# Optimization experiments

Hardware: AMD Instinct MI355X
Metric: run time of the kernel (lower is better)

Reference implementation:

```python
import jax, jax.numpy as jnp
import numpy as np

EPS = 1e-5  # torch BatchNorm1d default eps


def setup_inputs() -> dict:
    key = jax.random.key(0)
    ks = jax.random.split(key, 4)
    B, D, H, T = 1024, 256, 1024, 128
    s_ih = 1.0 / np.sqrt(H)
    return {
        "x": jax.random.normal(ks[0], (B, D), dtype=jnp.float32),
        "h0": jnp.zeros((B, H), dtype=jnp.float32),
        "W_ih": jax.random.normal(ks[1], (3 * H, D), dtype=jnp.float32) * s_ih,
        "W_hh": jax.random.normal(ks[2], (3 * H, H), dtype=jnp.float32) * s_ih,
        "b_ih": jnp.zeros((3 * H,), dtype=jnp.float32),
        "b_hh": jnp.zeros((3 * H,), dtype=jnp.float32),
        "W_lin": jax.random.normal(ks[3], (D, H), dtype=jnp.float32) * s_ih,
        "b_lin": jnp.zeros((D,), dtype=jnp.float32),
        "n_frames": T,
    }


def reference(x, h0, W_ih, W_hh, b_ih, b_hh, W_lin, b_lin, n_frames):
    H = h0.shape[-1]

    def step(carry, _):
        h, inp = carry
        gi = inp @ W_ih.T + b_ih          # (B, 3H)
        gh = h @ W_hh.T + b_hh            # (B, 3H)
        i_r, i_z, i_n = jnp.split(gi, 3, axis=-1)
        h_r, h_z, h_n = jnp.split(gh, 3, axis=-1)
        r = jax.nn.sigmoid(i_r + h_r)
        z = jax.nn.sigmoid(i_z + h_z)
        n = jnp.tanh(i_n + r * h_n)
        h_new = (1.0 - z) * n + z * h
        out = h_new @ W_lin.T + b_lin     # (B, D) -> next input
        return (h_new, out), out

    _, outs = jax.lax.scan(step, (h0, x), None, length=n_frames)  # (T, B, D)

    # BatchNorm1d(affine=False), training mode: per-frame batch statistics
    mean = outs.mean(axis=1, keepdims=True)
    var = outs.var(axis=1, keepdims=True)  # biased variance, as torch BN uses
    return (outs - mean) * jax.lax.rsqrt(var + EPS)
```

## Files before the change

kernel.cpp:

```cpp
#include <hip/hip_runtime.h>


#define DEVI __device__ __forceinline__

typedef __bf16 bf16x8 __attribute__((ext_vector_type(8)));
typedef float f32x4 __attribute__((ext_vector_type(4)));
typedef unsigned int u32x4 __attribute__((ext_vector_type(4)));

typedef __attribute__((address_space(1))) const unsigned int g_u32;
typedef __attribute__((address_space(3))) unsigned int l_u32;

DEVI unsigned short f2b(float f) {
  union { float f; unsigned u; } v; v.f = f;
  return (unsigned short)((v.u + 0x7fffu + ((v.u >> 16) & 1u)) >> 16);
}

DEVI void gl_lds16(const void* g, void* s) {
  __builtin_amdgcn_global_load_lds((g_u32*)g, (l_u32*)s, 16, 0, 0);
}
DEVI void st16_sc1(void* p, u32x4 v) {
  asm volatile("global_store_dwordx4 %0, %1, off sc1"
               :: "v"((unsigned long long)(__SIZE_TYPE__)p), "v"(v) : "memory");
}

DEVI float sigm(float x) { return 1.0f / (1.0f + __expf(-x)); }
DEVI float tanh_f(float x) {
  float t = __expf(-2.0f * fabsf(x));
  float r = (1.0f - t) / (1.0f + t);
  return x >= 0.0f ? r : -r;
}

__global__ __launch_bounds__(256, 2) void gru_persist(
    const unsigned short* __restrict__ XB,
    const unsigned short* __restrict__ WP0,
    const unsigned short* __restrict__ WP,
    const float* __restrict__ C0v,
    const float* __restrict__ CBv,
    const float* __restrict__ h0,
    unsigned short* __restrict__ HH,
    unsigned int* __restrict__ bar)
{
  __shared__ __align__(16) unsigned short As[3][64 * 64];
  __shared__ __align__(16) unsigned short Bs[3][128 * 64];
  __shared__ __align__(16) unsigned short Hs[64 * 32];
  const int tid = threadIdx.x;
  const int w = tid >> 6, lane = tid & 63;
  const int wr = w >> 1, wc = w & 1;
  const int srow = lane >> 3;
  const int schunk = (lane & 7) ^ srow;
  const int l15 = lane & 15, lg = lane >> 4;
  const int xb_ = blockIdx.x & 7, rb_ = blockIdx.x >> 3;
  const int mb = (xb_ >> 2) | ((rb_ & 7) << 1);
  const int nb = (xb_ & 3) | ((rb_ >> 3) << 2);
  const int j = nb * 32 + wc * 16 + l15;

  const float c0r = C0v[j], c0z = C0v[1024 + j], c0i = C0v[2048 + j], c0h = C0v[3072 + j];
  const float cbr = CBv[j], cbz = CBv[1024 + j], cbi = CBv[2048 + j], cbh = CBv[3072 + j];

  float hreg[2][4];
#pragma unroll
  for (int mi = 0; mi < 2; ++mi)
#pragma unroll
    for (int i = 0; i < 4; ++i)
      hreg[mi][i] = h0[(size_t)(mb * 64 + wr * 32 + mi * 16 + lg * 4 + i) * 1024 + j];

  int offA[2][2], offB[2][4];
#pragma unroll
  for (int kk = 0; kk < 2; ++kk) {
#pragma unroll
    for (int mi = 0; mi < 2; ++mi) {
      int rl = wr * 32 + mi * 16 + l15;
      int slot = (kk * 4 + lg) ^ (rl & 7);
      offA[kk][mi] = rl * 128 + slot * 16;
    }
#pragma unroll
    for (int g = 0; g < 4; ++g) {
      int cl = wc * 64 + g * 16 + l15;
      int slot = (kk * 4 + lg) ^ (cl & 7);
      offB[kk][g] = cl * 128 + slot * 16;
    }
  }
  const int offq0 = (0 * 8 + srow) * 1024 + schunk * 8;
  const int offq1 = (1 * 8 + srow) * 1024 + schunk * 8;
  const int offq2 = (2 * 8 + srow) * 1024 + schunk * 8;
  const int offq3 = (3 * 8 + srow) * 1024 + schunk * 8;
  const size_t arow_off = (size_t)(mb * 64 + w * 16) * 1024;
  const unsigned short* BrowS = WP + (size_t)(nb * 128 + w * 32) * 1024;
  const unsigned short* Arow0 = XB + (size_t)(mb * 64 + w * 16) * 256;
  const unsigned short* Brow0 = WP0 + (size_t)(nb * 128 + w * 32) * 256;

#define STAGE0(KT, BUF)                                                       \
  _Pragma("unroll")                                                           \
  for (int q = 0; q < 4; ++q)                                                 \
    gl_lds16(Brow0 + (size_t)(q * 8 + srow) * 256 + (KT) * 64 + schunk * 8,   \
             (char*)Bs[BUF] + (w * 32 + q * 8) * 128);                        \
  _Pragma("unroll")                                                           \
  for (int q = 0; q < 2; ++q)                                                 \
    gl_lds16(Arow0 + (size_t)(q * 8 + srow) * 256 + (KT) * 64 + schunk * 8,   \
             (char*)As[BUF] + (w * 16 + q * 8) * 128);
#define SSTAGE_B(KT, BUF)                                                     \
  gl_lds16(BrowS + offq0 + (KT) * 64, (char*)Bs[BUF] + (w * 32) * 128);       \
  gl_lds16(BrowS + offq1 + (KT) * 64, (char*)Bs[BUF] + (w * 32 + 8) * 128);   \
  gl_lds16(BrowS + offq2 + (KT) * 64, (char*)Bs[BUF] + (w * 32 + 16) * 128);  \
  gl_lds16(BrowS + offq3 + (KT) * 64, (char*)Bs[BUF] + (w * 32 + 24) * 128);
#define SSTAGE_A(KT, BUF)                                                     \
  gl_lds16(ArowS + offq0 + (KT) * 64, (char*)As[BUF] + (w * 16) * 128);       \
  gl_lds16(ArowS + offq1 + (KT) * 64, (char*)As[BUF] + (w * 16 + 8) * 128);

  for (int t = 0; t < 128; ++t) {
    const bool first = (t == 0);
    const int iters = first ? 4 : 16;
    const unsigned short* ArowS =
        HH + (((size_t)(first ? 0 : t - 1)) << 20) + arow_off;

    f32x4 acc[2][4] = {};

    if (first) {
      STAGE0(0, 0)
      STAGE0(1, 1)
    } else {
      SSTAGE_A(0, 0)
      SSTAGE_A(1, 1)
    }
    int cur = 0, pre = 2;
    for (int kt = 0; kt < iters; ++kt) {
      if (kt == 0) {
        if (first) asm volatile("s_waitcnt vmcnt(6)" ::: "memory");
        else       asm volatile("s_waitcnt vmcnt(2)" ::: "memory");
      } else if (kt == iters - 1) {
        asm volatile("s_waitcnt vmcnt(0)" ::: "memory");
      } else {
        asm volatile("s_waitcnt vmcnt(6)" ::: "memory");
      }
      __builtin_amdgcn_s_barrier();
      if (kt + 2 < iters) {
        if (first) { STAGE0(kt + 2, pre) }
        else       { SSTAGE_B(kt + 2, pre) SSTAGE_A(kt + 2, pre) }
      }
      __builtin_amdgcn_s_setprio(1);
#pragma unroll
      for (int kk = 0; kk < 2; ++kk) {
        bf16x8 a[2], b[4];
        const char* Ab = (const char*)As[cur];
        const char* Bb = (const char*)Bs[cur];
#pragma unroll
        for (int mi = 0; mi < 2; ++mi)
          a[mi] = *(const bf16x8*)(Ab + offA[kk][mi]);
#pragma unroll
        for (int g = 0; g < 4; ++g)
          b[g] = *(const bf16x8*)(Bb + offB[kk][g]);
#pragma unroll
        for (int mi = 0; mi < 2; ++mi)
#pragma unroll
          for (int g = 0; g < 4; ++g)
            acc[mi][g] = __builtin_amdgcn_mfma_f32_16x16x32_bf16(
                a[mi], b[g], acc[mi][g], 0, 0, 0);
      }
      __builtin_amdgcn_s_setprio(0);
      cur = (cur == 2) ? 0 : cur + 1;
      pre = (pre == 2) ? 0 : pre + 1;
    }

    const float cr = first ? c0r : cbr, cz = first ? c0z : cbz;
    const float ci = first ? c0i : cbi, ch = first ? c0h : cbh;
#pragma unroll
    for (int mi = 0; mi < 2; ++mi)
#pragma unroll
      for (int i = 0; i < 4; ++i) {
        float rg = sigm(acc[mi][0][i] + cr);
        float zg = sigm(acc[mi][1][i] + cz);
        float ng = tanh_f(acc[mi][2][i] + ci + rg * (acc[mi][3][i] + ch));
        float h = (1.0f - zg) * ng + zg * hreg[mi][i];
        hreg[mi][i] = h;
        Hs[(wr * 32 + mi * 16 + lg * 4 + i) * 32 + wc * 16 + l15] = f2b(h);
      }
    __syncthreads();
    {
      const int row = tid >> 2, part = tid & 3;
      u32x4 v = *(const u32x4*)((char*)Hs + tid * 16);
      size_t off = (size_t)(mb * 64 + row) * 1024 + nb * 32 + part * 8;
      st16_sc1(HH + ((size_t)t << 20) + off, v);
    }

    if (t != 127) {
      SSTAGE_B(0, 0)
      SSTAGE_B(1, 1)
      asm volatile("s_waitcnt vmcnt(8)" ::: "memory");
      __syncthreads();
      if (tid == 0)
        __hip_atomic_store(&bar[mb * 32 + nb], (unsigned)(t + 1),
                           __ATOMIC_RELAXED, __HIP_MEMORY_SCOPE_AGENT);
      if (w == 0) {
        const unsigned tgt = (unsigned)(t + 1);
        for (;;) {
          unsigned v = __hip_atomic_load(&bar[mb * 32 + (lane & 31)],
                                         __ATOMIC_RELAXED,
                                         __HIP_MEMORY_SCOPE_AGENT);
          if (__all((int)(v >= tgt))) break;
          __builtin_amdgcn_s_sleep(1);
        }
      }
      __syncthreads();
    }
  }
#undef STAGE0
#undef SSTAGE_A
#undef SSTAGE_B
}

__global__ __launch_bounds__(256) void outgemm(
    const unsigned short* __restrict__ A,
    const unsigned short* __restrict__ Bw,
    const float* __restrict__ bias,
    float* __restrict__ out)
{
  __shared__ __align__(16) unsigned short As[128 * 64];
  __shared__ __align__(16) unsigned short Bs[128 * 64];
  const int tid = threadIdx.x;
  const int w = tid >> 6, lane = tid & 63;
  const int srow = lane >> 3, schunk = (lane & 7) ^ srow;
  const int l15 = lane & 15, lg = lane >> 4;
  const int mb = blockIdx.x >> 1, nb = blockIdx.x & 1;
  const int wr = w >> 1, wc = w & 1;
  f32x4 acc[4][4] = {};
  const unsigned short* Ag = A + (size_t)(mb * 128 + w * 32) * 1024;
  const unsigned short* Bg = Bw + (size_t)(nb * 128 + w * 32) * 1024;
  for (int kt = 0; kt < 16; ++kt) {
    const int k0 = kt * 64;
    __syncthreads();
#pragma unroll
    for (int q = 0; q < 4; ++q) {
      gl_lds16(Ag + (size_t)(q * 8 + srow) * 1024 + k0 + schunk * 8,
               (char*)As + (w * 32 + q * 8) * 128);
      gl_lds16(Bg + (size_t)(q * 8 + srow) * 1024 + k0 + schunk * 8,
               (char*)Bs + (w * 32 + q * 8) * 128);
    }
    __syncthreads();
#pragma unroll
    for (int kk = 0; kk < 2; ++kk) {
      bf16x8 a[4], b[4];
#pragma unroll
      for (int mi = 0; mi < 4; ++mi) {
        int rl = wr * 64 + mi * 16 + l15;
        int slot = (kk * 4 + lg) ^ (rl & 7);
        a[mi] = *(const bf16x8*)(As + rl * 64 + slot * 8);
      }
#pragma unroll
      for (int g = 0; g < 4; ++g) {
        int cl = g * 32 + wc * 16 + l15;
        int slot = (kk * 4 + lg) ^ (cl & 7);
        b[g] = *(const bf16x8*)(Bs + cl * 64 + slot * 8);
      }
#pragma unroll
      for (int mi = 0; mi < 4; ++mi)
#pragma unroll
        for (int g = 0; g < 4; ++g)
          acc[mi][g] = __builtin_amdgcn_mfma_f32_16x16x32_bf16(
              a[mi], b[g], acc[mi][g], 0, 0, 0);
    }
  }
#pragma unroll
  for (int mi = 0; mi < 4; ++mi)
#pragma unroll
    for (int g = 0; g < 4; ++g) {
      int d = nb * 128 + g * 32 + wc * 16 + l15;
      float bb = bias[d];
#pragma unroll
      for (int i = 0; i < 4; ++i) {
        int row = mb * 128 + wr * 64 + mi * 16 + lg * 4 + i;
        out[(size_t)row * 256 + d] = acc[mi][g][i] + bb;
      }
    }
}

__global__ __launch_bounds__(256) void gemm128(
    const unsigned short* __restrict__ A, const unsigned short* __restrict__ B,
    float* __restrict__ C, int K, int nT)
{
  __shared__ __align__(16) unsigned short As[128 * 64];
  __shared__ __align__(16) unsigned short Bs[128 * 64];
  const int tid = threadIdx.x;
  const int w = tid >> 6, lane = tid & 63;
  const int srow = lane >> 3, schunk = (lane & 7) ^ srow;
  const int l15 = lane & 15, lg = lane >> 4;
  const int mb = blockIdx.x / nT, nb = blockIdx.x % nT;
  const int wr = w >> 1, wc = w & 1;
  const int N = nT * 128;
  f32x4 acc[4][4] = {};
  const unsigned short* Ag = A + (size_t)(mb * 128 + w * 32) * K;
  const unsigned short* Bg = B + (size_t)(nb * 128 + w * 32) * K;
  for (int kt = 0; kt < (K >> 6); ++kt) {
    const int k0 = kt * 64;
    __syncthreads();
#pragma unroll
    for (int q = 0; q < 4; ++q) {
      gl_lds16(Ag + (size_t)(q * 8 + srow) * K + k0 + schunk * 8,
               (char*)As + (w * 32 + q * 8) * 128);
      gl_lds16(Bg + (size_t)(q * 8 + srow) * K + k0 + schunk * 8,
               (char*)Bs + (w * 32 + q * 8) * 128);
    }
    __syncthreads();
#pragma unroll
    for (int kk = 0; kk < 2; ++kk) {
      bf16x8 a[4], b[4];
#pragma unroll
      for (int mi = 0; mi < 4; ++mi) {
        int rl = wr * 64 + mi * 16 + l15;
        int slot = (kk * 4 + lg) ^ (rl & 7);
        a[mi] = *(const bf16x8*)(As + rl * 64 + slot * 8);
      }
#pragma unroll
      for (int g = 0; g < 4; ++g) {
        int cl = g * 32 + wc * 16 + l15;
        int slot = (kk * 4 + lg) ^ (cl & 7);
        b[g] = *(const bf16x8*)(Bs + cl * 64 + slot * 8);
      }
#pragma unroll
      for (int mi = 0; mi < 4; ++mi)
#pragma unroll
        for (int g = 0; g < 4; ++g)
          acc[mi][g] = __builtin_amdgcn_mfma_f32_16x16x32_bf16(
              a[mi], b[g], acc[mi][g], 0, 0, 0);
    }
  }
#pragma unroll
  for (int mi = 0; mi < 4; ++mi)
#pragma unroll
    for (int g = 0; g < 4; ++g)
#pragma unroll
      for (int i = 0; i < 4; ++i)
        C[(size_t)(mb * 128 + wr * 64 + mi * 16 + lg * 4 + i) * N + nb * 128 +
          g * 32 + wc * 16 + l15] = acc[mi][g][i];
}

__global__ void castall(const float* __restrict__ x, const float* __restrict__ wih,
                        const float* __restrict__ wlin, unsigned short* __restrict__ xb,
                        unsigned short* __restrict__ wihb, unsigned short* __restrict__ wlb) {
  int i = blockIdx.x * 256 + threadIdx.x;
  if (i < 262144) { xb[i] = f2b(x[i]); wlb[i] = f2b(wlin[i]); }
  if (i < 786432) wihb[i] = f2b(wih[i]);
}

__global__ void tcast(const float* __restrict__ in, unsigned short* __restrict__ out) {
  __shared__ float t[32][33];
  int i0 = blockIdx.x * 32, d0 = blockIdx.y * 32;
  for (int r = threadIdx.y; r < 32; r += 8)
    t[r][threadIdx.x] = in[(size_t)(d0 + r) * 1024 + i0 + threadIdx.x];
  __syncthreads();
  for (int r = threadIdx.y; r < 32; r += 8)
    out[(size_t)(i0 + r) * 256 + d0 + threadIdx.x] = f2b(t[threadIdx.x][r]);
}

__global__ void asmWp(const float* __restrict__ CMT, const float* __restrict__ Whh,
                      unsigned short* __restrict__ Wp) {
  int col = blockIdx.x;
  int jt = col >> 7, L = col & 127;
  int ch = L >> 6, gate = (L >> 4) & 3, c0 = L & 15;
  int j = jt * 32 + ch * 16 + c0;
  const float* s1;
  const float* s2 = nullptr;
  if (gate == 0)      { s1 = CMT + (size_t)j * 1024;          s2 = Whh + (size_t)j * 1024; }
  else if (gate == 1) { s1 = CMT + (size_t)(1024 + j) * 1024; s2 = Whh + (size_t)(1024 + j) * 1024; }
  else if (gate == 2) { s1 = CMT + (size_t)(2048 + j) * 1024; }
  else                { s1 = Whh + (size_t)(2048 + j) * 1024; }
  unsigned short* dst = Wp + (size_t)col * 1024;
  for (int k = threadIdx.x; k < 1024; k += 256) {
    float v = s1[k] + (s2 ? s2[k] : 0.0f);
    dst[k] = f2b(v);
  }
}

__global__ void asmWp0(const float* __restrict__ Wih, unsigned short* __restrict__ Wp0) {
  int col = blockIdx.x;
  int jt = col >> 7, L = col & 127;
  int ch = L >> 6, gate = (L >> 4) & 3, c0 = L & 15;
  int j = jt * 32 + ch * 16 + c0;
  int d = threadIdx.x;
  float v = 0.0f;
  if (gate < 3) v = Wih[(size_t)(gate * 1024 + j) * 256 + d];
  Wp0[(size_t)col * 256 + d] = f2b(v);
}

__global__ void biask(const float* __restrict__ Wih, const float* __restrict__ bih,
                      const float* __restrict__ bhh, const float* __restrict__ blin,
                      float* __restrict__ cbig, float* __restrict__ c0) {
  int j = blockIdx.x * 256 + threadIdx.x;
  if (j >= 1024) return;
  float bli[3];
  for (int g = 0; g < 3; ++g) {
    int gg = g * 1024 + j;
    float s = bih[gg];
    const float* wrow = Wih + (size_t)gg * 256;
    for (int d = 0; d < 256; ++d) s += blin[d] * wrow[d];
    bli[g] = s;
  }
  cbig[j] = bli[0] + bhh[j];
  cbig[1024 + j] = bli[1] + bhh[1024 + j];
  cbig[2048 + j] = bli[2];
  cbig[3072 + j] = bhh[2048 + j];
  c0[j] = bih[j] + bhh[j];
  c0[1024 + j] = bih[1024 + j] + bhh[1024 + j];
  c0[2048 + j] = bih[2048 + j];
  c0[3072 + j] = bhh[2048 + j];
}

__global__ void bnstats(const float* __restrict__ o, float* __restrict__ mean,
                        float* __restrict__ rstd) {
  int t = blockIdx.x;
  int d = threadIdx.x & 255;
  int bq = threadIdx.x >> 8;
  const float* base = o + (size_t)t * 1024 * 256;
  float s = 0.0f, ss = 0.0f;
  for (int b = bq * 256; b < bq * 256 + 256; ++b) {
    float v = base[(size_t)b * 256 + d];
    s += v; ss += v * v;
  }
  __shared__ float S[4][256], SS[4][256];
  S[bq][d] = s; SS[bq][d] = ss;
  __syncthreads();
  if (threadIdx.x < 256) {
    float st = S[0][d] + S[1][d] + S[2][d] + S[3][d];
    float sst = SS[0][d] + SS[1][d] + SS[2][d] + SS[3][d];
    float m = st * (1.0f / 1024.0f);
    float var = sst * (1.0f / 1024.0f) - m * m;
    mean[t * 256 + d] = m;
    rstd[t * 256 + d] = rsqrtf(var + 1e-5f);
  }
}

__global__ void bnnorm(float* __restrict__ o, const float* __restrict__ mean,
                       const float* __restrict__ rstd) {
  size_t base = ((size_t)blockIdx.x * 256 + threadIdx.x) * 4;
  int t = (int)(base >> 18);
  int d = (int)(base & 255);
  float4 v = *(float4*)(o + base);
  const float* mp = mean + t * 256 + d;
  const float* rp = rstd + t * 256 + d;
  float4 r;
  r.x = (v.x - mp[0]) * rp[0];
  r.y = (v.y - mp[1]) * rp[1];
  r.z = (v.z - mp[2]) * rp[2];
  r.w = (v.w - mp[3]) * rp[3];
  *(float4*)(o + base) = r;
}

extern "C" void kernel_launch(void* const* d_in, const int* in_sizes, int n_in,
                              void* d_out, int out_size, void* d_ws, size_t ws_size,
                              hipStream_t stream) {
  (void)in_sizes; (void)n_in; (void)out_size; (void)ws_size;
  const float* x    = (const float*)d_in[0];
  const float* h0   = (const float*)d_in[1];
  const float* Wih  = (const float*)d_in[2];
  const float* Whh  = (const float*)d_in[3];
  const float* bih  = (const float*)d_in[4];
  const float* bhh  = (const float*)d_in[5];
  const float* Wlin = (const float*)d_in[6];
  const float* blin = (const float*)d_in[7];
  float* out = (float*)d_out;

  char* ws = (char*)d_ws;
  size_t off = 0;
  auto alloc = [&](size_t bytes) {
    char* p = ws + off;
    off += (bytes + 255) & ~(size_t)255;
    return p;
  };
  unsigned short* WP   = (unsigned short*)alloc(4096ull * 1024 * 2);
  unsigned short* WP0  = (unsigned short*)alloc(4096ull * 256 * 2);
  unsigned short* WIHB = (unsigned short*)alloc(3072ull * 256 * 2);
  unsigned short* WLT  = (unsigned short*)alloc(1024ull * 256 * 2);
  unsigned short* WLB  = (unsigned short*)alloc(256ull * 1024 * 2);
  unsigned short* XB   = (unsigned short*)alloc(1024ull * 256 * 2);
  float* CMT  = (float*)alloc(3072ull * 1024 * 4);
  float* CBIG = (float*)alloc(4096 * 4);
  float* C0   = (float*)alloc(4096 * 4);
  unsigned short* HH  = (unsigned short*)alloc(128ull * 1024 * 1024 * 2);
  float* MEAN = (float*)alloc(128 * 256 * 4);
  float* RSTD = (float*)alloc(128 * 256 * 4);
  unsigned int* BAR = (unsigned int*)alloc(4096);

  (void)hipMemsetAsync(BAR, 0, 4096, stream);

  castall<<<3072, 256, 0, stream>>>(x, Wih, Wlin, XB, WIHB, WLB);
  tcast<<<dim3(32, 8), dim3(32, 8), 0, stream>>>(Wlin, WLT);
  gemm128<<<192, 256, 0, stream>>>(WIHB, WLT, CMT, 256, 8);
  asmWp<<<4096, 256, 0, stream>>>(CMT, Whh, WP);
  asmWp0<<<4096, 256, 0, stream>>>(Wih, WP0);
  biask<<<4, 256, 0, stream>>>(Wih, bih, bhh, blin, CBIG, C0);

  gru_persist<<<512, 256, 0, stream>>>(XB, WP0, WP, C0, CBIG, h0, HH, BAR);

  outgemm<<<2048, 256, 0, stream>>>(HH, WLB, blin, out);

  bnstats<<<128, 1024, 0, stream>>>(out, MEAN, RSTD);
  bnnorm<<<32768, 256, 0, stream>>>(out, MEAN, RSTD);
}
```

Baseline: 2.023 ms.

## Use 128x128 tiles with split-K across wave halves in persistent GRU kernel

The persistent GRU kernel moves from 512 blocks of 256 threads with 64x128 tiles to 256 blocks of 512 threads with 128-row tiles. The two halves of the waves each handle half of every K slice, and their partial accumulators are reduced through shared memory before the gate math. This halves the number of blocks taking part in the per-step grid barrier and raises operand reuse per block. In exchange it adds an LDS reduction and extra syncthreads every timestep, and only half the waves do the gate math.

```diff
diff --git a/kernel.cpp b/kernel.cpp
--- a/kernel.cpp
+++ b/kernel.cpp
@@ -30,7 +30,7 @@
   return x >= 0.0f ? r : -r;
 }
 
-__global__ __launch_bounds__(256, 2) void gru_persist(
+__global__ __launch_bounds__(512, 2) void gru_persist(
     const unsigned short* __restrict__ XB,
     const unsigned short* __restrict__ WP0,
     const unsigned short* __restrict__ WP,
@@ -40,80 +40,74 @@
     unsigned short* __restrict__ HH,
     unsigned int* __restrict__ bar)
 {
-  __shared__ __align__(16) unsigned short As[3][64 * 64];
-  __shared__ __align__(16) unsigned short Bs[3][128 * 64];
-  __shared__ __align__(16) unsigned short Hs[64 * 32];
+  __shared__ __align__(16) unsigned short smem[53248];
+  unsigned short* const Asb = smem;
+  unsigned short* const Bsb = smem + 24576;
+  unsigned short* const Hs  = smem + 49152;
+
   const int tid = threadIdx.x;
   const int w = tid >> 6, lane = tid & 63;
-  const int wr = w >> 1, wc = w & 1;
+  const int tw = w & 3, kh = w >> 2;
+  const int twr = tw >> 1, twc = tw & 1;
   const int srow = lane >> 3;
   const int schunk = (lane & 7) ^ srow;
   const int l15 = lane & 15, lg = lane >> 4;
   const int xb_ = blockIdx.x & 7, rb_ = blockIdx.x >> 3;
-  const int mb = (xb_ >> 2) | ((rb_ & 7) << 1);
-  const int nb = (xb_ & 3) | ((rb_ >> 3) << 2);
-  const int j = nb * 32 + wc * 16 + l15;
-
-  const float c0r = C0v[j], c0z = C0v[1024 + j], c0i = C0v[2048 + j], c0h = C0v[3072 + j];
-  const float cbr = CBv[j], cbz = CBv[1024 + j], cbi = CBv[2048 + j], cbh = CBv[3072 + j];
-
-  float hreg[2][4];
-#pragma unroll
-  for (int mi = 0; mi < 2; ++mi)
-#pragma unroll
-    for (int i = 0; i < 4; ++i)
-      hreg[mi][i] = h0[(size_t)(mb * 64 + wr * 32 + mi * 16 + lg * 4 + i) * 1024 + j];
-
-  int offA[2][2], offB[2][4];
-#pragma unroll
-  for (int kk = 0; kk < 2; ++kk) {
-#pragma unroll
-    for (int mi = 0; mi < 2; ++mi) {
-      int rl = wr * 32 + mi * 16 + l15;
-      int slot = (kk * 4 + lg) ^ (rl & 7);
-      offA[kk][mi] = rl * 128 + slot * 16;
-    }
-#pragma unroll
-    for (int g = 0; g < 4; ++g) {
-      int cl = wc * 64 + g * 16 + l15;
-      int slot = (kk * 4 + lg) ^ (cl & 7);
-      offB[kk][g] = cl * 128 + slot * 16;
-    }
-  }
-  const int offq0 = (0 * 8 + srow) * 1024 + schunk * 8;
-  const int offq1 = (1 * 8 + srow) * 1024 + schunk * 8;
-  const int offq2 = (2 * 8 + srow) * 1024 + schunk * 8;
-  const int offq3 = (3 * 8 + srow) * 1024 + schunk * 8;
-  const size_t arow_off = (size_t)(mb * 64 + w * 16) * 1024;
-  const unsigned short* BrowS = WP + (size_t)(nb * 128 + w * 32) * 1024;
-  const unsigned short* Arow0 = XB + (size_t)(mb * 64 + w * 16) * 256;
-  const unsigned short* Brow0 = WP0 + (size_t)(nb * 128 + w * 32) * 256;
+  const int mb = rb_ & 7;
+  const int nb = xb_ | ((rb_ >> 3) << 3);
+  const int j = nb * 32 + twc * 16 + l15;
+
+  float c0r = 0, c0z = 0, c0i = 0, c0h = 0, cbr = 0, cbz = 0, cbi = 0, cbh = 0;
+  if (kh == 0) {
+    c0r = C0v[j]; c0z = C0v[1024 + j]; c0i = C0v[2048 + j]; c0h = C0v[3072 + j];
+    cbr = CBv[j]; cbz = CBv[1024 + j]; cbi = CBv[2048 + j]; cbh = CBv[3072 + j];
+  }
+
+  float hreg[4][4];
+  if (kh == 0) {
+#pragma unroll
+    for (int mi = 0; mi < 4; ++mi)
+#pragma unroll
+      for (int i = 0; i < 4; ++i)
+        hreg[mi][i] =
+            h0[(size_t)(mb * 128 + twr * 64 + mi * 16 + lg * 4 + i) * 1024 + j];
+  }
+
+  const int slot = ((kh << 2) | lg) ^ (l15 & 7);
+  int offA[4], offB[4];
+#pragma unroll
+  for (int q = 0; q < 4; ++q) {
+    offA[q] = (twr * 64 + q * 16 + l15) * 128 + slot * 16;
+    offB[q] = (twc * 64 + q * 16 + l15) * 128 + slot * 16;
+  }
+  const int offq0 = srow * 1024 + schunk * 8;
+  const int offq1 = (8 + srow) * 1024 + schunk * 8;
+  const int offp0 = srow * 256 + schunk * 8;
+  const int offp1 = (8 + srow) * 256 + schunk * 8;
+  const size_t arow_off = (size_t)(mb * 128 + w * 16) * 1024;
+  const unsigned short* BrowS = WP + (size_t)(nb * 128 + w * 16) * 1024;
+  const unsigned short* Arow0 = XB + (size_t)(mb * 128 + w * 16) * 256;
+  const unsigned short* Brow0 = WP0 + (size_t)(nb * 128 + w * 16) * 256;
+  float* const scr = (float*)smem + (tw < 3 ? tw * 4096 : 20480);
 
 #define STAGE0(KT, BUF)                                                       \
-  _Pragma("unroll")                                                           \
-  for (int q = 0; q < 4; ++q)                                                 \
-    gl_lds16(Brow0 + (size_t)(q * 8 + srow) * 256 + (KT) * 64 + schunk * 8,   \
-             (char*)Bs[BUF] + (w * 32 + q * 8) * 128);                        \
-  _Pragma("unroll")                                                           \
-  for (int q = 0; q < 2; ++q)                                                 \
-    gl_lds16(Arow0 + (size_t)(q * 8 + srow) * 256 + (KT) * 64 + schunk * 8,   \
-             (char*)As[BUF] + (w * 16 + q * 8) * 128);
+  gl_lds16(Brow0 + offp0 + (KT) * 64, (char*)Bsb + (BUF) * 16384 + (w * 16) * 128);     \
+  gl_lds16(Brow0 + offp1 + (KT) * 64, (char*)Bsb + (BUF) * 16384 + (w * 16 + 8) * 128); \
+  gl_lds16(Arow0 + offp0 + (KT) * 64, (char*)Asb + (BUF) * 16384 + (w * 16) * 128);     \
+  gl_lds16(Arow0 + offp1 + (KT) * 64, (char*)Asb + (BUF) * 16384 + (w * 16 + 8) * 128);
 #define SSTAGE_B(KT, BUF)                                                     \
-  gl_lds16(BrowS + offq0 + (KT) * 64, (char*)Bs[BUF] + (w * 32) * 128);       \
-  gl_lds16(BrowS + offq1 + (KT) * 64, (char*)Bs[BUF] + (w * 32 + 8) * 128);   \
-  gl_lds16(BrowS + offq2 + (KT) * 64, (char*)Bs[BUF] + (w * 32 + 16) * 128);  \
-  gl_lds16(BrowS + offq3 + (KT) * 64, (char*)Bs[BUF] + (w * 32 + 24) * 128);
+  gl_lds16(BrowS + offq0 + (KT) * 64, (char*)Bsb + (BUF) * 16384 + (w * 16) * 128);     \
+  gl_lds16(BrowS + offq1 + (KT) * 64, (char*)Bsb + (BUF) * 16384 + (w * 16 + 8) * 128);
 #define SSTAGE_A(KT, BUF)                                                     \
-  gl_lds16(ArowS + offq0 + (KT) * 64, (char*)As[BUF] + (w * 16) * 128);       \
-  gl_lds16(ArowS + offq1 + (KT) * 64, (char*)As[BUF] + (w * 16 + 8) * 128);
+  gl_lds16(ArowS + offq0 + (KT) * 64, (char*)Asb + (BUF) * 16384 + (w * 16) * 128);     \
+  gl_lds16(ArowS + offq1 + (KT) * 64, (char*)Asb + (BUF) * 16384 + (w * 16 + 8) * 128);
 
   for (int t = 0; t < 128; ++t) {
     const bool first = (t == 0);
     const int iters = first ? 4 : 16;
-    const unsigned short* ArowS =
-        HH + (((size_t)(first ? 0 : t - 1)) << 20) + arow_off;
-
-    f32x4 acc[2][4] = {};
+    const unsigned short* ArowS = HH + (((size_t)(first ? 0 : t - 1)) << 20) + arow_off;
+
+    f32x4 acc[4][4] = {};
 
     if (first) {
       STAGE0(0, 0)
@@ -125,12 +119,12 @@
     int cur = 0, pre = 2;
     for (int kt = 0; kt < iters; ++kt) {
       if (kt == 0) {
-        if (first) asm volatile("s_waitcnt vmcnt(6)" ::: "memory");
+        if (first) asm volatile("s_waitcnt vmcnt(4)" ::: "memory");
         else       asm volatile("s_waitcnt vmcnt(2)" ::: "memory");
       } else if (kt == iters - 1) {
         asm volatile("s_waitcnt vmcnt(0)" ::: "memory");
       } else {
-        asm volatile("s_waitcnt vmcnt(6)" ::: "memory");
+        asm volatile("s_waitcnt vmcnt(4)" ::: "memory");
       }
       __builtin_amdgcn_s_barrier();
       if (kt + 2 < iters) {
@@ -138,19 +132,16 @@
         else       { SSTAGE_B(kt + 2, pre) SSTAGE_A(kt + 2, pre) }
       }
       __builtin_amdgcn_s_setprio(1);
-#pragma unroll
-      for (int kk = 0; kk < 2; ++kk) {
-        bf16x8 a[2], b[4];
-        const char* Ab = (const char*)As[cur];
-        const char* Bb = (const char*)Bs[cur];
-#pragma unroll
-        for (int mi = 0; mi < 2; ++mi)
-          a[mi] = *(const bf16x8*)(Ab + offA[kk][mi]);
-#pragma unroll
-        for (int g = 0; g < 4; ++g)
-          b[g] = *(const bf16x8*)(Bb + offB[kk][g]);
-#pragma unroll
-        for (int mi = 0; mi < 2; ++mi)
+      {
+        bf16x8 a[4], b[4];
+        const char* Ab = (const char*)Asb + cur * 16384;
+        const char* Bb = (const char*)Bsb + cur * 16384;
+#pragma unroll
+        for (int mi = 0; mi < 4; ++mi) a[mi] = *(const bf16x8*)(Ab + offA[mi]);
+#pragma unroll
+        for (int g = 0; g < 4; ++g)    b[g] = *(const bf16x8*)(Bb + offB[g]);
+#pragma unroll
+        for (int mi = 0; mi < 4; ++mi)
 #pragma unroll
           for (int g = 0; g < 4; ++g)
             acc[mi][g] = __builtin_amdgcn_mfma_f32_16x16x32_bf16(
@@ -161,31 +152,46 @@
       pre = (pre == 2) ? 0 : pre + 1;
     }
 
-    const float cr = first ? c0r : cbr, cz = first ? c0z : cbz;
-    const float ci = first ? c0i : cbi, ch = first ? c0h : cbh;
-#pragma unroll
-    for (int mi = 0; mi < 2; ++mi)
-#pragma unroll
-      for (int i = 0; i < 4; ++i) {
-        float rg = sigm(acc[mi][0][i] + cr);
-        float zg = sigm(acc[mi][1][i] + cz);
-        float ng = tanh_f(acc[mi][2][i] + ci + rg * (acc[mi][3][i] + ch));
-        float h = (1.0f - zg) * ng + zg * hreg[mi][i];
-        hreg[mi][i] = h;
-        Hs[(wr * 32 + mi * 16 + lg * 4 + i) * 32 + wc * 16 + l15] = f2b(h);
-      }
+    __syncthreads();
+    if (kh == 1) {
+#pragma unroll
+      for (int mi = 0; mi < 4; ++mi)
+#pragma unroll
+        for (int g = 0; g < 4; ++g)
+          *(f32x4*)(scr + (mi * 4 + g) * 256 + lane * 4) = acc[mi][g];
+    }
+    __syncthreads();
+    if (kh == 0) {
+      const float cr = first ? c0r : cbr, cz = first ? c0z : cbz;
+      const float ci = first ? c0i : cbi, ch = first ? c0h : cbh;
+#pragma unroll
+      for (int mi = 0; mi < 4; ++mi) {
+#pragma unroll
+        for (int g = 0; g < 4; ++g)
+          acc[mi][g] += *(const f32x4*)(scr + (mi * 4 + g) * 256 + lane * 4);
+#pragma unroll
+        for (int i = 0; i < 4; ++i) {
+          float rg = sigm(acc[mi][0][i] + cr);
+          float zg = sigm(acc[mi][1][i] + cz);
+          float ng = tanh_f(acc[mi][2][i] + ci + rg * (acc[mi][3][i] + ch));
+          float h = (1.0f - zg) * ng + zg * hreg[mi][i];
+          hreg[mi][i] = h;
+          Hs[(twr * 64 + mi * 16 + lg * 4 + i) * 32 + twc * 16 + l15] = f2b(h);
+        }
+      }
+    }
     __syncthreads();
     {
       const int row = tid >> 2, part = tid & 3;
       u32x4 v = *(const u32x4*)((char*)Hs + tid * 16);
-      size_t off = (size_t)(mb * 64 + row) * 1024 + nb * 32 + part * 8;
+      size_t off = (size_t)(mb * 128 + row) * 1024 + nb * 32 + part * 8;
       st16_sc1(HH + ((size_t)t << 20) + off, v);
     }
 
     if (t != 127) {
       SSTAGE_B(0, 0)
       SSTAGE_B(1, 1)
-      asm volatile("s_waitcnt vmcnt(8)" ::: "memory");
+      asm volatile("s_waitcnt vmcnt(4)" ::: "memory");
       __syncthreads();
       if (tid == 0)
         __hip_atomic_store(&bar[mb * 32 + nb], (unsigned)(t + 1),
@@ -488,7 +494,7 @@
   asmWp0<<<4096, 256, 0, stream>>>(Wih, WP0);
   biask<<<4, 256, 0, stream>>>(Wih, bih, bhh, blin, CBIG, C0);
 
-  gru_persist<<<512, 256, 0, stream>>>(XB, WP0, WP, C0, CBIG, h0, HH, BAR);
+  gru_persist<<<256, 512, 0, stream>>>(XB, WP0, WP, C0, CBIG, h0, HH, BAR);
 
   outgemm<<<2048, 256, 0, stream>>>(HH, WLB, blin, out);
 
```

New measurement: 2.080 ms. 2.8% more time.

## Split grid barrier per K-half and fuse BN statistics into output GEMM epilogue

Applied to the files above, without the earlier changes.

The persistent GRU kernel no longer waits for all 32 column blocks before the next step. It waits only on the lower-half flags, prefetches the first A tiles right away, and checks the upper-half flags mid-loop at k-tile 6, so barrier latency overlaps with MFMA work. The wait is now done by every wave with cache-bypassing loads rather than one wave followed by a __syncthreads. Separately, the output GEMM epilogue accumulates per-frame sums and sums of squares with shuffles and atomics, so a tiny finalize kernel replaces the bnstats pass that re-read the whole output. This adds atomic contention, makes the summation order nondeterministic, and relies on subtle memory ordering in the split barrier.

```diff
diff --git a/kernel.cpp b/kernel.cpp
--- a/kernel.cpp
+++ b/kernel.cpp
@@ -21,6 +21,25 @@
 DEVI void st16_sc1(void* p, u32x4 v) {
   asm volatile("global_store_dwordx4 %0, %1, off sc1"
                :: "v"((unsigned long long)(__SIZE_TYPE__)p), "v"(v) : "memory");
+}
+DEVI unsigned ld_flag(const unsigned* p) {
+  unsigned v;
+  asm volatile("global_load_dword %0, %1, off sc0 sc1"
+               : "=v"(v) : "v"((unsigned long long)(__SIZE_TYPE__)p) : "memory");
+  return v;
+}
+DEVI void vm0_pin(unsigned& v) {
+  asm volatile("s_waitcnt vmcnt(0)" ::: "memory");
+  __builtin_amdgcn_sched_barrier(0);
+  asm volatile("" : "+v"(v));
+}
+DEVI void spin_flags(const unsigned* p, unsigned tgt) {
+  for (;;) {
+    unsigned v = ld_flag(p);
+    vm0_pin(v);
+    if (__all((int)(v >= tgt))) return;
+    __builtin_amdgcn_s_sleep(1);
+  }
 }
 
 DEVI float sigm(float x) { return 1.0f / (1.0f + __expf(-x)); }
@@ -80,14 +99,16 @@
       offB[kk][g] = cl * 128 + slot * 16;
     }
   }
-  const int offq0 = (0 * 8 + srow) * 1024 + schunk * 8;
-  const int offq1 = (1 * 8 + srow) * 1024 + schunk * 8;
-  const int offq2 = (2 * 8 + srow) * 1024 + schunk * 8;
-  const int offq3 = (3 * 8 + srow) * 1024 + schunk * 8;
+  const int offq0 = srow * 1024 + schunk * 8;
+  const int offq1 = (8 + srow) * 1024 + schunk * 8;
+  const int offq2 = (16 + srow) * 1024 + schunk * 8;
+  const int offq3 = (24 + srow) * 1024 + schunk * 8;
   const size_t arow_off = (size_t)(mb * 64 + w * 16) * 1024;
   const unsigned short* BrowS = WP + (size_t)(nb * 128 + w * 32) * 1024;
   const unsigned short* Arow0 = XB + (size_t)(mb * 64 + w * 16) * 256;
   const unsigned short* Brow0 = WP0 + (size_t)(nb * 128 + w * 32) * 256;
+  const unsigned* flo = bar + mb * 32 + (lane & 15);
+  const unsigned* fhi = bar + mb * 32 + 16 + (lane & 15);
 
 #define STAGE0(KT, BUF)                                                       \
   _Pragma("unroll")                                                           \
@@ -103,62 +124,66 @@
   gl_lds16(BrowS + offq1 + (KT) * 64, (char*)Bs[BUF] + (w * 32 + 8) * 128);   \
   gl_lds16(BrowS + offq2 + (KT) * 64, (char*)Bs[BUF] + (w * 32 + 16) * 128);  \
   gl_lds16(BrowS + offq3 + (KT) * 64, (char*)Bs[BUF] + (w * 32 + 24) * 128);
-#define SSTAGE_A(KT, BUF)                                                     \
-  gl_lds16(ArowS + offq0 + (KT) * 64, (char*)As[BUF] + (w * 16) * 128);       \
-  gl_lds16(ArowS + offq1 + (KT) * 64, (char*)As[BUF] + (w * 16 + 8) * 128);
+#define SSTAGE_A(KT, BUF, PTR)                                                \
+  gl_lds16(PTR + offq0 + (KT) * 64, (char*)As[BUF] + (w * 16) * 128);         \
+  gl_lds16(PTR + offq1 + (KT) * 64, (char*)As[BUF] + (w * 16 + 8) * 128);
+
+#define MFMA_CLUSTER                                                          \
+  __builtin_amdgcn_s_setprio(1);                                              \
+  {                                                                           \
+    const char* Ab = (const char*)As[cur];                                    \
+    const char* Bb = (const char*)Bs[cur];                                    \
+    _Pragma("unroll")                                                         \
+    for (int kk = 0; kk < 2; ++kk) {                                          \
+      bf16x8 a[2], b[4];                                                      \
+      _Pragma("unroll")                                                       \
+      for (int mi = 0; mi < 2; ++mi) a[mi] = *(const bf16x8*)(Ab + offA[kk][mi]); \
+      _Pragma("unroll")                                                       \
+      for (int g = 0; g < 4; ++g) b[g] = *(const bf16x8*)(Bb + offB[kk][g]);  \
+      _Pragma("unroll")                                                       \
+      for (int mi = 0; mi < 2; ++mi)                                          \
+        _Pragma("unroll")                                                     \
+        for (int g = 0; g < 4; ++g)                                           \
+          acc[mi][g] = __builtin_amdgcn_mfma_f32_16x16x32_bf16(               \
+              a[mi], b[g], acc[mi][g], 0, 0, 0);                              \
+    }                                                                         \
+  }                                                                           \
+  __builtin_amdgcn_s_setprio(0);
 
   for (int t = 0; t < 128; ++t) {
     const bool first = (t == 0);
-    const int iters = first ? 4 : 16;
-    const unsigned short* ArowS =
-        HH + (((size_t)(first ? 0 : t - 1)) << 20) + arow_off;
-
     f32x4 acc[2][4] = {};
+    int cur = 0, pre = 2;
 
     if (first) {
       STAGE0(0, 0)
       STAGE0(1, 1)
+      for (int kt = 0; kt < 4; ++kt) {
+        if (kt < 3) asm volatile("s_waitcnt vmcnt(6)" ::: "memory");
+        else        asm volatile("s_waitcnt vmcnt(0)" ::: "memory");
+        __builtin_amdgcn_s_barrier();
+        if (kt + 2 < 4) { STAGE0(kt + 2, pre) }
+        MFMA_CLUSTER
+        cur = (cur == 2) ? 0 : cur + 1;
+        pre = (pre == 2) ? 0 : pre + 1;
+      }
     } else {
-      SSTAGE_A(0, 0)
-      SSTAGE_A(1, 1)
-    }
-    int cur = 0, pre = 2;
-    for (int kt = 0; kt < iters; ++kt) {
-      if (kt == 0) {
-        if (first) asm volatile("s_waitcnt vmcnt(6)" ::: "memory");
-        else       asm volatile("s_waitcnt vmcnt(2)" ::: "memory");
-      } else if (kt == iters - 1) {
-        asm volatile("s_waitcnt vmcnt(0)" ::: "memory");
-      } else {
-        asm volatile("s_waitcnt vmcnt(6)" ::: "memory");
-      }
-      __builtin_amdgcn_s_barrier();
-      if (kt + 2 < iters) {
-        if (first) { STAGE0(kt + 2, pre) }
-        else       { SSTAGE_B(kt + 2, pre) SSTAGE_A(kt + 2, pre) }
-      }
-      __builtin_amdgcn_s_setprio(1);
-#pragma unroll
-      for (int kk = 0; kk < 2; ++kk) {
-        bf16x8 a[2], b[4];
-        const char* Ab = (const char*)As[cur];
-        const char* Bb = (const char*)Bs[cur];
-#pragma unroll
-        for (int mi = 0; mi < 2; ++mi)
-          a[mi] = *(const bf16x8*)(Ab + offA[kk][mi]);
-#pragma unroll
-        for (int g = 0; g < 4; ++g)
-          b[g] = *(const bf16x8*)(Bb + offB[kk][g]);
-#pragma unroll
-        for (int mi = 0; mi < 2; ++mi)
-#pragma unroll
-          for (int g = 0; g < 4; ++g)
-            acc[mi][g] = __builtin_amdgcn_mfma_f32_16x16x32_bf16(
-                a[mi], b[g], acc[mi][g], 0, 0, 0);
-      }
-      __builtin_amdgcn_s_setprio(0);
-      cur = (cur == 2) ? 0 : cur + 1;
-      pre = (pre == 2) ? 0 : pre + 1;
+      const unsigned short* ArowS = HH + (((size_t)(t - 1)) << 20) + arow_off;
+      for (int kt = 0; kt < 16; ++kt) {
+        if (kt == 0)       asm volatile("s_waitcnt vmcnt(2)" ::: "memory");
+        else if (kt < 15)  asm volatile("s_waitcnt vmcnt(6)" ::: "memory");
+        else               asm volatile("s_waitcnt vmcnt(0)" ::: "memory");
+        __builtin_amdgcn_s_barrier();
+        if (kt == 6) {
+          unsigned fhv = ld_flag(fhi);
+          vm0_pin(fhv);
+          if (!__all((int)(fhv >= (unsigned)t))) spin_flags(fhi, (unsigned)t);
+        }
+        if (kt + 2 < 16) { SSTAGE_B(kt + 2, pre) SSTAGE_A(kt + 2, pre, ArowS) }
+        MFMA_CLUSTER
+        cur = (cur == 2) ? 0 : cur + 1;
+        pre = (pre == 2) ? 0 : pre + 1;
+      }
     }
 
     const float cr = first ? c0r : cbr, cz = first ? c0z : cbz;
@@ -190,29 +215,29 @@
       if (tid == 0)
         __hip_atomic_store(&bar[mb * 32 + nb], (unsigned)(t + 1),
                            __ATOMIC_RELAXED, __HIP_MEMORY_SCOPE_AGENT);
-      if (w == 0) {
-        const unsigned tgt = (unsigned)(t + 1);
-        for (;;) {
-          unsigned v = __hip_atomic_load(&bar[mb * 32 + (lane & 31)],
-                                         __ATOMIC_RELAXED,
-                                         __HIP_MEMORY_SCOPE_AGENT);
-          if (__all((int)(v >= tgt))) break;
-          __builtin_amdgcn_s_sleep(1);
-        }
-      }
-      __syncthreads();
+      unsigned flv = ld_flag(flo);
+      vm0_pin(flv);
+      if (!__all((int)(flv >= (unsigned)(t + 1)))) spin_flags(flo, (unsigned)(t + 1));
+      {
+        const unsigned short* ArowN = HH + ((size_t)t << 20) + arow_off;
+        SSTAGE_A(0, 0, ArowN)
+        SSTAGE_A(1, 1, ArowN)
+      }
     }
   }
 #undef STAGE0
 #undef SSTAGE_A
 #undef SSTAGE_B
+#undef MFMA_CLUSTER
 }
 
 __global__ __launch_bounds__(256) void outgemm(
     const unsigned short* __restrict__ A,
     const unsigned short* __restrict__ Bw,
     const float* __restrict__ bias,
-    float* __restrict__ out)
+    float* __restrict__ out,
+    float* __restrict__ sumv,
+    float* __restrict__ sumsq)
 {
   __shared__ __align__(16) unsigned short As[128 * 64];
   __shared__ __align__(16) unsigned short Bs[128 * 64];
@@ -259,6 +284,8 @@
               a[mi], b[g], acc[mi][g], 0, 0, 0);
     }
   }
+  const int tf = mb >> 3;
+  float s[4] = {0, 0, 0, 0}, ss[4] = {0, 0, 0, 0};
 #pragma unroll
   for (int mi = 0; mi < 4; ++mi)
 #pragma unroll
@@ -268,9 +295,24 @@
 #pragma unroll
       for (int i = 0; i < 4; ++i) {
         int row = mb * 128 + wr * 64 + mi * 16 + lg * 4 + i;
-        out[(size_t)row * 256 + d] = acc[mi][g][i] + bb;
-      }
-    }
+        float v = acc[mi][g][i] + bb;
+        out[(size_t)row * 256 + d] = v;
+        s[g] += v; ss[g] += v * v;
+      }
+    }
+#pragma unroll
+  for (int g = 0; g < 4; ++g) {
+    s[g] += __shfl_xor(s[g], 16);  s[g] += __shfl_xor(s[g], 32);
+    ss[g] += __shfl_xor(ss[g], 16); ss[g] += __shfl_xor(ss[g], 32);
+  }
+  if (lg == 0) {
+#pragma unroll
+    for (int g = 0; g < 4; ++g) {
+      int d = nb * 128 + g * 32 + wc * 16 + l15;
+      atomicAdd(&sumv[tf * 256 + d], s[g]);
+      atomicAdd(&sumsq[tf * 256 + d], ss[g]);
+    }
+  }
 }
 
 __global__ __launch_bounds__(256) void gemm128(
@@ -404,28 +446,13 @@
   c0[3072 + j] = bhh[2048 + j];
 }
 
-__global__ void bnstats(const float* __restrict__ o, float* __restrict__ mean,
-                        float* __restrict__ rstd) {
-  int t = blockIdx.x;
-  int d = threadIdx.x & 255;
-  int bq = threadIdx.x >> 8;
-  const float* base = o + (size_t)t * 1024 * 256;
-  float s = 0.0f, ss = 0.0f;
-  for (int b = bq * 256; b < bq * 256 + 256; ++b) {
-    float v = base[(size_t)b * 256 + d];
-    s += v; ss += v * v;
-  }
-  __shared__ float S[4][256], SS[4][256];
-  S[bq][d] = s; SS[bq][d] = ss;
-  __syncthreads();
-  if (threadIdx.x < 256) {
-    float st = S[0][d] + S[1][d] + S[2][d] + S[3][d];
-    float sst = SS[0][d] + SS[1][d] + SS[2][d] + SS[3][d];
-    float m = st * (1.0f / 1024.0f);
-    float var = sst * (1.0f / 1024.0f) - m * m;
-    mean[t * 256 + d] = m;
-    rstd[t * 256 + d] = rsqrtf(var + 1e-5f);
-  }
+__global__ void bnfin(const float* __restrict__ sv, const float* __restrict__ sq,
+                      float* __restrict__ mean, float* __restrict__ rstd) {
+  int i = blockIdx.x * 256 + threadIdx.x;
+  float m = sv[i] * (1.0f / 1024.0f);
+  float var = sq[i] * (1.0f / 1024.0f) - m * m;
+  mean[i] = m;
+  rstd[i] = rsqrtf(var + 1e-5f);
 }
 
 __global__ void bnnorm(float* __restrict__ o, const float* __restrict__ mean,
@@ -475,11 +502,14 @@
   float* CBIG = (float*)alloc(4096 * 4);
   float* C0   = (float*)alloc(4096 * 4);
   unsigned short* HH  = (unsigned short*)alloc(128ull * 1024 * 1024 * 2);
+  float* SUMV = (float*)alloc(128 * 256 * 4);
+  float* SUMSQ= (float*)alloc(128 * 256 * 4);
   float* MEAN = (float*)alloc(128 * 256 * 4);
   float* RSTD = (float*)alloc(128 * 256 * 4);
   unsigned int* BAR = (unsigned int*)alloc(4096);
 
   (void)hipMemsetAsync(BAR, 0, 4096, stream);
+  (void)hipMemsetAsync(SUMV, 0, 2 * 128 * 256 * 4, stream);
 
   castall<<<3072, 256, 0, stream>>>(x, Wih, Wlin, XB, WIHB, WLB);
   tcast<<<dim3(32, 8), dim3(32, 8), 0, stream>>>(Wlin, WLT);
@@ -490,8 +520,8 @@
 
   gru_persist<<<512, 256, 0, stream>>>(XB, WP0, WP, C0, CBIG, h0, HH, BAR);
 
-  outgemm<<<2048, 256, 0, stream>>>(HH, WLB, blin, out);
-
-  bnstats<<<128, 1024, 0, stream>>>(out, MEAN, RSTD);
+  outgemm<<<2048, 256, 0, stream>>>(HH, WLB, blin, out, SUMV, SUMSQ);
+
+  bnfin<<<128, 256, 0, stream>>>(SUMV, SUMSQ, MEAN, RSTD);
   bnnorm<<<32768, 256, 0, stream>>>(out, MEAN, RSTD);
 }
```

After: 2.243 ms. 1.11x slower.
